# Kernel optimization log

Hardware: AMD Instinct MI355X
Metric: run time of the kernel (lower is better)

Reference implementation:

```python
import jax, jax.numpy as jnp
import numpy as np

# Module config (matches init_kwargs)
N_HEADS = 32        # query heads
MAX_SEQLEN = 2048
LOCAL_BLOCKS = 16
VERT_STRIDE = 8
BLOCK_SIZE = 64
HEAD_SIZE = 128
KV_HEADS = 8
BATCH = 2
SEQLEN = 1024       # per-sample length (equal-length varlen batch)


def _dense_sparse_mask(maxlen):
    """Local + strided block-sparse causal mask, heterogeneous heads.
    Returns bool [N_HEADS, maxlen, maxlen]; True = attend."""
    nb = MAX_SEQLEN // BLOCK_SIZE
    q_pos = jnp.arange(nb)[:, None]
    k_pos = jnp.arange(nb)[None, :]
    h = jnp.arange(N_HEADS)[:, None]
    # head-dependent vertical stride (homo_head=False)
    vert = ((jnp.arange(nb)[None, :] + h + 1) % VERT_STRIDE == 0)  # [H, nb]
    blk = (q_pos >= k_pos) & (((q_pos - k_pos) < LOCAL_BLOCKS)[None] | vert[:, None, :])  # [H, nb, nb]
    tok = jnp.repeat(jnp.repeat(blk, BLOCK_SIZE, axis=1), BLOCK_SIZE, axis=2)  # [H, S, S]
    causal = jnp.tril(jnp.ones((MAX_SEQLEN, MAX_SEQLEN), dtype=bool))
    tok = tok & causal[None]
    return tok[:, :maxlen, :maxlen]


def setup_inputs() -> dict:
    key = jax.random.key(0)
    kq, kk, kv = jax.random.split(key, 3)
    total = BATCH * SEQLEN
    q = jax.random.normal(kq, (total, N_HEADS, HEAD_SIZE), dtype=jnp.float32)
    k = jax.random.normal(kk, (total, KV_HEADS, HEAD_SIZE), dtype=jnp.float32)
    v = jax.random.normal(kv, (total, KV_HEADS, HEAD_SIZE), dtype=jnp.float32)
    cu_seqlens_k = jnp.arange(BATCH + 1, dtype=jnp.int32) * SEQLEN  # [0, 1024, 2048]
    return {"q": q, "k": k, "v": v, "cu_seqlens_k": cu_seqlens_k}


def reference(q, k, v, cu_seqlens_k):
    B = cu_seqlens_k.shape[0] - 1
    T, Hq, D = q.shape
    Hk = k.shape[1]
    r = Hq // Hk                      # q/kv head ratio (GQA)
    L = T // B                        # equal-length sequences
    scale = 1.0 / np.sqrt(D)

    mask = _dense_sparse_mask(L)      # [Hq, L, L]
    bias = jnp.where(mask, jnp.float32(0.0), jnp.finfo(jnp.float32).min)
    bias = bias.reshape(Hk, r, L, L)

    qb = q.reshape(B, L, Hk, r, D)
    kb = k.reshape(B, L, Hk, D)
    vb = v.reshape(B, L, Hk, D)

    scores = jnp.einsum('bqgrd,bkgd->bgrqk', qb, kb) * scale  # [B, Hk, r, L, L]
    attn = jax.nn.softmax(scores + bias[None], axis=-1)
    out = jnp.einsum('bgrqk,bkgd->bqgrd', attn, vb)           # [B, L, Hk, r, D]
    return out.reshape(T, Hq, D)
```

## Files before the change

### kernel.cpp

```cpp
#include <hip/hip_runtime.h>

typedef __attribute__((ext_vector_type(8))) short s8bf;
typedef __attribute__((ext_vector_type(4))) float f4;
typedef __attribute__((ext_vector_type(2))) unsigned u2;
typedef __attribute__((ext_vector_type(4))) unsigned u4;

#define HQ 32
#define HK 8
#define DH 128

static __device__ __forceinline__ unsigned cvtpk(float a, float b) {
  unsigned r;
  asm("v_cvt_pk_bf16_f32 %0, %1, %2" : "=v"(r) : "v"(a), "v"(b));
  return r;
}
union frag_u { s8bf v; unsigned u[4]; };

static __device__ __forceinline__ void gload_lds16(const short* g, short* l) {
  __builtin_amdgcn_global_load_lds(
      (const __attribute__((address_space(1))) void*)g,
      (__attribute__((address_space(3))) void*)l, 16, 0, 0);
}

#define WAIT_VM(N)                                         \
  do {                                                     \
    asm volatile("s_waitcnt vmcnt(" #N ")" ::: "memory");  \
    __builtin_amdgcn_sched_barrier(0);                     \
  } while (0)


__global__ void prep_kernel(const float* __restrict__ kg, const float* __restrict__ vg,
                            short* __restrict__ kbt, short* __restrict__ vbt) {
  const int blk = blockIdx.x;
  if (blk < 512) {
    const int gid = blk * 256 + threadIdx.x;
#pragma unroll
    for (int i = 0; i < 2; ++i) {
      int c = gid + i * 131072;
      int l16 = c & 15, quad = (c >> 4) & 3;
      int f = (c >> 6) & 15;
      int kt = (c >> 10) & 15;
      int bg = c >> 14;
      int b = bg >> 3, g = bg & 7;
      int key = kt * 64 + (f >> 2) * 16 + l16;
      int d0 = (f & 3) * 32 + quad * 8;
      const float* src = kg + (((size_t)(b * 1024 + key) * HK + g) * DH + d0);
      f4 a = *(const f4*)src, cc = *(const f4*)(src + 4);
      u4 w;
      w[0] = cvtpk(a[0], a[1]);   w[1] = cvtpk(a[2], a[3]);
      w[2] = cvtpk(cc[0], cc[1]); w[3] = cvtpk(cc[2], cc[3]);
      *(u4*)(kbt + (size_t)c * 8) = w;
    }
  } else {
    __shared__ short T[32 * 130];
    const int t = blk - 512;
    const int half = t & 1, tile = t >> 1;
    const int bg = tile >> 4, kt = tile & 15;
    const int b = bg >> 3, g = bg & 7;
#pragma unroll
    for (int i = 0; i < 4; ++i) {
      int e = threadIdx.x * 4 + i * 1024;
      int key = e >> 7, d = e & 127;
      f4 x = *(const f4*)(vg + (((size_t)(b * 1024 + kt * 64 + half * 32 + key) * HK + g) * DH + d));
      u2 w; w[0] = cvtpk(x[0], x[1]); w[1] = cvtpk(x[2], x[3]);
      *(u2*)&T[key * 130 + d] = w;
    }
    __syncthreads();
    short* dst = vbt + (size_t)(bg * 16 + kt) * 8192;
#pragma unroll
    for (int i = 0; i < 2; ++i) {
      int c = threadIdx.x + i * 256;
      int lane = c & 63, dt = c >> 6;
      int fidx = dt * 2 + half;
      int l16 = lane & 15, quad = (lane >> 4) & 3;
      int d = dt * 16 + l16;
      int k0 = quad * 4;
      int k1 = k0 + 16;
      u4 w;
      w[0] = (unsigned)(unsigned short)T[(k0 + 0) * 130 + d] |
             ((unsigned)(unsigned short)T[(k0 + 1) * 130 + d] << 16);
      w[1] = (unsigned)(unsigned short)T[(k0 + 2) * 130 + d] |
             ((unsigned)(unsigned short)T[(k0 + 3) * 130 + d] << 16);
      w[2] = (unsigned)(unsigned short)T[(k1 + 0) * 130 + d] |
             ((unsigned)(unsigned short)T[(k1 + 1) * 130 + d] << 16);
      w[3] = (unsigned)(unsigned short)T[(k1 + 2) * 130 + d] |
             ((unsigned)(unsigned short)T[(k1 + 3) * 130 + d] << 16);
      *(u4*)(dst + (size_t)(fidx * 64 + lane) * 8) = w;
    }
  }
}

__launch_bounds__(256, 4)
__global__ void fa_main(const float* __restrict__ qg, const short* __restrict__ kbt,
                        const short* __restrict__ vbt, float* __restrict__ out) {
  const int id  = blockIdx.x;
  const int g   = id & 7;
  const int s   = id >> 3;
  const int qt  = 15 - (s >> 3);
  const int rem = s & 7;
  const int b   = rem >> 2;
  const int h   = g * 4 + (rem & 3);
  const int bg  = b * 8 + g;
  const int kmax = 2 * qt + 1;

  const int tid  = threadIdx.x;
  const int wave = tid >> 6, lane = tid & 63;
  const int l16  = lane & 15, quad = lane >> 4;
  const int qlocal = wave * 16 + l16;
  const int seq0 = b * 1024;

  __shared__ short smem[2][8192];

  const float qmul = 0.08838834764831845f * 1.4426950408889634f;
  const float* qp = qg + ((size_t)(seq0 + qt * 64 + qlocal) * HQ + h) * DH;
  s8bf qf[4];
#pragma unroll
  for (int dk = 0; dk < 4; ++dk) {
    const float* p = qp + dk * 32 + quad * 8;
    f4 a = *(const f4*)p, c = *(const f4*)(p + 4);
    frag_u t;
    t.u[0] = cvtpk(a[0] * qmul, a[1] * qmul);
    t.u[1] = cvtpk(a[2] * qmul, a[3] * qmul);
    t.u[2] = cvtpk(c[0] * qmul, c[1] * qmul);
    t.u[3] = cvtpk(c[2] * qmul, c[3] * qmul);
    qf[dk] = t.v;
  }

  float l_ = 0.0f;
  f4 oacc[8];
#pragma unroll
  for (int dt = 0; dt < 8; ++dt) oacc[dt] = (f4)(0.0f);

  const short* ktile = kbt + (size_t)bg * 16 * 8192;
  const short* vtile = vbt + (size_t)bg * 16 * 8192;

  __builtin_amdgcn_sched_barrier(0);

#define STAGE_TILE(J, BUF)                                                             \
  do {                                                                                 \
    const short* kb32 = ktile + (size_t)((J) >> 1) * 8192 + ((J) & 1) * 4096;          \
    const short* vb32 = vtile + (size_t)((J) >> 1) * 8192 + ((J) & 1) * 512;           \
    _Pragma("unroll")                                                                  \
    for (int i = 0; i < 4; ++i) {                                                      \
      int fidx = wave * 4 + i;                                                         \
      if (fidx < 8) {                                                                  \
        gload_lds16(kb32 + (size_t)(fidx * 64 + lane) * 8, &smem[BUF][fidx * 512]);    \
      } else {                                                                         \
        gload_lds16(vb32 + (size_t)((fidx - 8) * 128 + lane) * 8,                      \
                    &smem[BUF][4096 + (fidx - 8) * 512]);                              \
      }                                                                                \
    }                                                                                  \
  } while (0)

  STAGE_TILE(0, 0);

  for (int kt = 0; kt <= kmax; ++kt) {
    const int cur = kt & 1;

    if (kt < kmax) {
      STAGE_TILE(kt + 1, cur ^ 1);
      WAIT_VM(4);
    } else {
      WAIT_VM(0);
    }
    __builtin_amdgcn_s_barrier();
    __builtin_amdgcn_sched_barrier(0);

    const short* kb = &smem[cur][lane * 8];
    const short* vb = &smem[cur][4096 + lane * 8];

    f4 sacc[2];
#pragma unroll
    for (int ct = 0; ct < 2; ++ct) sacc[ct] = (f4)(0.0f);
    __builtin_amdgcn_s_setprio(1);
#pragma unroll
    for (int dk = 0; dk < 4; ++dk)
#pragma unroll
      for (int ct = 0; ct < 2; ++ct) {
        s8bf kf = *(const s8bf*)&kb[(ct * 4 + dk) * 512];
        sacc[ct] = __builtin_amdgcn_mfma_f32_16x16x32_bf16(kf, qf[dk], sacc[ct], 0, 0, 0);
      }
    __builtin_amdgcn_s_setprio(0);

    if (kt >= 2 * qt) {
      int thr = qlocal - (kt - 2 * qt) * 32;
#pragma unroll
      for (int ct = 0; ct < 2; ++ct)
#pragma unroll
        for (int i = 0; i < 4; ++i) {
          int key = ct * 16 + quad * 4 + i;
          if (key > thr) sacc[ct][i] = -1e30f;
        }
    }

    float rs = 0.0f;
    frag_u fr;
#pragma unroll
    for (int ct = 0; ct < 2; ++ct) {
      float p0 = exp2f(fminf(sacc[ct][0], 30.0f));
      float p1 = exp2f(fminf(sacc[ct][1], 30.0f));
      float p2 = exp2f(fminf(sacc[ct][2], 30.0f));
      float p3 = exp2f(fminf(sacc[ct][3], 30.0f));
      rs += (p0 + p1) + (p2 + p3);
      fr.u[ct * 2 + 0] = cvtpk(p0, p1);
      fr.u[ct * 2 + 1] = cvtpk(p2, p3);
    }
    l_ += rs;

    __builtin_amdgcn_s_setprio(1);
#pragma unroll
    for (int dt = 0; dt < 8; ++dt) {
      s8bf vf = *(const s8bf*)&vb[dt * 512];
      oacc[dt] = __builtin_amdgcn_mfma_f32_16x16x32_bf16(vf, fr.v, oacc[dt], 0, 0, 0);
    }
    __builtin_amdgcn_s_setprio(0);

    asm volatile("s_waitcnt lgkmcnt(0)" ::: "memory");
    __builtin_amdgcn_sched_barrier(0);
    __builtin_amdgcn_s_barrier();
  }

  float lt = l_;
  lt += __shfl_xor(lt, 16);
  lt += __shfl_xor(lt, 32);
  float inv = 1.0f / lt;
  float* op = out + ((size_t)(seq0 + qt * 64 + qlocal) * HQ + h) * DH;
#pragma unroll
  for (int dt = 0; dt < 8; ++dt) {
    f4 w;
    w[0] = oacc[dt][0] * inv; w[1] = oacc[dt][1] * inv;
    w[2] = oacc[dt][2] * inv; w[3] = oacc[dt][3] * inv;
    *(f4*)(op + dt * 16 + quad * 4) = w;
  }
}

extern "C" void kernel_launch(void* const* d_in, const int* in_sizes, int n_in,
                              void* d_out, int out_size, void* d_ws, size_t ws_size,
                              hipStream_t stream) {
  const float* q = (const float*)d_in[0];
  const float* k = (const float*)d_in[1];
  const float* v = (const float*)d_in[2];
  float* out = (float*)d_out;

  short* kbt = (short*)d_ws;
  short* vbt = kbt + (size_t)16 * 16 * 8192;

  prep_kernel<<<dim3(1024), 256, 0, stream>>>(k, v, kbt, vbt);
  fa_main<<<dim3(1024), 256, 0, stream>>>(q, kbt, vbt, out);
}
```

Baseline: 125.2 us.

## Software-pipeline QK^T of next tile with softmax and PV of current tile

```diff
diff --git a/kernel.cpp b/kernel.cpp
--- a/kernel.cpp
+++ b/kernel.cpp
@@ -90,7 +90,7 @@
   }
 }
 
-__launch_bounds__(256, 4)
+__launch_bounds__(256, 3)
 __global__ void fa_main(const float* __restrict__ qg, const short* __restrict__ kbt,
                         const short* __restrict__ vbt, float* __restrict__ out) {
   const int id  = blockIdx.x;
@@ -109,7 +109,7 @@
   const int qlocal = wave * 16 + l16;
   const int seq0 = b * 1024;
 
-  __shared__ short smem[2][8192];
+  __shared__ short smem[3][8192];
 
   const float qmul = 0.08838834764831845f * 1.4426950408889634f;
   const float* qp = qg + ((size_t)(seq0 + qt * 64 + qlocal) * HQ + h) * DH;
@@ -152,72 +152,91 @@
     }                                                                                  \
   } while (0)
 
+#define COMPUTE_S(SACC, BUF, J)                                                        \
+  do {                                                                                 \
+    const short* kb = &smem[BUF][lane * 8];                                            \
+    _Pragma("unroll")                                                                  \
+    for (int ct = 0; ct < 2; ++ct) (SACC)[ct] = (f4)(0.0f);                            \
+    __builtin_amdgcn_s_setprio(1);                                                     \
+    _Pragma("unroll")                                                                  \
+    for (int dk = 0; dk < 4; ++dk)                                                     \
+      _Pragma("unroll")                                                                \
+      for (int ct = 0; ct < 2; ++ct) {                                                 \
+        s8bf kf = *(const s8bf*)&kb[(ct * 4 + dk) * 512];                              \
+        (SACC)[ct] = __builtin_amdgcn_mfma_f32_16x16x32_bf16(kf, qf[dk], (SACC)[ct], 0, 0, 0); \
+      }                                                                                \
+    __builtin_amdgcn_s_setprio(0);                                                     \
+    if ((J) >= 2 * qt) {                                                               \
+      int thr = qlocal - ((J) - 2 * qt) * 32;                                          \
+      _Pragma("unroll")                                                                \
+      for (int ct = 0; ct < 2; ++ct)                                                   \
+        _Pragma("unroll")                                                              \
+        for (int i = 0; i < 4; ++i) {                                                  \
+          int key = ct * 16 + quad * 4 + i;                                            \
+          if (key > thr) (SACC)[ct][i] = -1e30f;                                       \
+        }                                                                              \
+    }                                                                                  \
+  } while (0)
+
   STAGE_TILE(0, 0);
-
-  for (int kt = 0; kt <= kmax; ++kt) {
-    const int cur = kt & 1;
-
-    if (kt < kmax) {
-      STAGE_TILE(kt + 1, cur ^ 1);
-      WAIT_VM(4);
-    } else {
-      WAIT_VM(0);
-    }
-    __builtin_amdgcn_s_barrier();
-    __builtin_amdgcn_sched_barrier(0);
-
-    const short* kb = &smem[cur][lane * 8];
-    const short* vb = &smem[cur][4096 + lane * 8];
-
-    f4 sacc[2];
-#pragma unroll
-    for (int ct = 0; ct < 2; ++ct) sacc[ct] = (f4)(0.0f);
-    __builtin_amdgcn_s_setprio(1);
-#pragma unroll
-    for (int dk = 0; dk < 4; ++dk)
-#pragma unroll
-      for (int ct = 0; ct < 2; ++ct) {
-        s8bf kf = *(const s8bf*)&kb[(ct * 4 + dk) * 512];
-        sacc[ct] = __builtin_amdgcn_mfma_f32_16x16x32_bf16(kf, qf[dk], sacc[ct], 0, 0, 0);
-      }
-    __builtin_amdgcn_s_setprio(0);
-
-    if (kt >= 2 * qt) {
-      int thr = qlocal - (kt - 2 * qt) * 32;
-#pragma unroll
-      for (int ct = 0; ct < 2; ++ct)
-#pragma unroll
-        for (int i = 0; i < 4; ++i) {
-          int key = ct * 16 + quad * 4 + i;
-          if (key > thr) sacc[ct][i] = -1e30f;
-        }
+  WAIT_VM(0);
+  __builtin_amdgcn_s_barrier();
+  __builtin_amdgcn_sched_barrier(0);
+  STAGE_TILE(1, 1);
+
+  f4 saccC[2];
+  COMPUTE_S(saccC, 0, 0);
+
+  for (int t = 0; t <= kmax; ++t) {
+    const int bc = t % 3;
+
+    s8bf vfr[8];
+    {
+      const short* vb = &smem[bc][4096 + lane * 8];
+#pragma unroll
+      for (int dt = 0; dt < 8; ++dt) vfr[dt] = *(const s8bf*)&vb[dt * 512];
     }
 
     float rs = 0.0f;
     frag_u fr;
 #pragma unroll
     for (int ct = 0; ct < 2; ++ct) {
-      float p0 = exp2f(fminf(sacc[ct][0], 30.0f));
-      float p1 = exp2f(fminf(sacc[ct][1], 30.0f));
-      float p2 = exp2f(fminf(sacc[ct][2], 30.0f));
-      float p3 = exp2f(fminf(sacc[ct][3], 30.0f));
+      float p0 = exp2f(fminf(saccC[ct][0], 30.0f));
+      float p1 = exp2f(fminf(saccC[ct][1], 30.0f));
+      float p2 = exp2f(fminf(saccC[ct][2], 30.0f));
+      float p3 = exp2f(fminf(saccC[ct][3], 30.0f));
       rs += (p0 + p1) + (p2 + p3);
       fr.u[ct * 2 + 0] = cvtpk(p0, p1);
       fr.u[ct * 2 + 1] = cvtpk(p2, p3);
     }
     l_ += rs;
 
+    f4 saccN[2];
+    if (t < kmax) {
+      if (t + 2 <= kmax) {
+        STAGE_TILE(t + 2, (t + 2) % 3);
+        WAIT_VM(4);
+      } else {
+        WAIT_VM(0);
+      }
+      __builtin_amdgcn_s_barrier();
+      __builtin_amdgcn_sched_barrier(0);
+      COMPUTE_S(saccN, (t + 1) % 3, t + 1);
+    }
+
     __builtin_amdgcn_s_setprio(1);
 #pragma unroll
-    for (int dt = 0; dt < 8; ++dt) {
-      s8bf vf = *(const s8bf*)&vb[dt * 512];
-      oacc[dt] = __builtin_amdgcn_mfma_f32_16x16x32_bf16(vf, fr.v, oacc[dt], 0, 0, 0);
-    }
+    for (int dt = 0; dt < 8; ++dt)
+      oacc[dt] = __builtin_amdgcn_mfma_f32_16x16x32_bf16(vfr[dt], fr.v, oacc[dt], 0, 0, 0);
     __builtin_amdgcn_s_setprio(0);
 
-    asm volatile("s_waitcnt lgkmcnt(0)" ::: "memory");
-    __builtin_amdgcn_sched_barrier(0);
-    __builtin_amdgcn_s_barrier();
+    if (t < kmax) {
+      asm volatile("s_waitcnt lgkmcnt(0)" ::: "memory");
+      __builtin_amdgcn_sched_barrier(0);
+      __builtin_amdgcn_s_barrier();
+      saccC[0] = saccN[0];
+      saccC[1] = saccN[1];
+    }
   }
 
   float lt = l_;
```

Result: slower. 129.1 us (+3.1%).

## Split key range across two wave groups per block and merge partials via LDS

Applied to the files above, without the earlier changes.

```diff
diff --git a/kernel.cpp b/kernel.cpp
--- a/kernel.cpp
+++ b/kernel.cpp
@@ -90,7 +90,7 @@
   }
 }
 
-__launch_bounds__(256, 4)
+__launch_bounds__(512, 4)
 __global__ void fa_main(const float* __restrict__ qg, const short* __restrict__ kbt,
                         const short* __restrict__ vbt, float* __restrict__ out) {
   const int id  = blockIdx.x;
@@ -101,15 +101,15 @@
   const int b   = rem >> 2;
   const int h   = g * 4 + (rem & 3);
   const int bg  = b * 8 + g;
-  const int kmax = 2 * qt + 1;
 
   const int tid  = threadIdx.x;
   const int wave = tid >> 6, lane = tid & 63;
+  const int half = wave >> 2, wsub = wave & 3;
   const int l16  = lane & 15, quad = lane >> 4;
-  const int qlocal = wave * 16 + l16;
+  const int qlocal = wsub * 16 + l16;
   const int seq0 = b * 1024;
 
-  __shared__ short smem[2][8192];
+  __shared__ short smem[2][2][8192];
 
   const float qmul = 0.08838834764831845f * 1.4426950408889634f;
   const float* qp = qg + ((size_t)(seq0 + qt * 64 + qlocal) * HQ + h) * DH;
@@ -142,23 +142,27 @@
     const short* vb32 = vtile + (size_t)((J) >> 1) * 8192 + ((J) & 1) * 512;           \
     _Pragma("unroll")                                                                  \
     for (int i = 0; i < 4; ++i) {                                                      \
-      int fidx = wave * 4 + i;                                                         \
+      int fidx = wsub * 4 + i;                                                         \
       if (fidx < 8) {                                                                  \
-        gload_lds16(kb32 + (size_t)(fidx * 64 + lane) * 8, &smem[BUF][fidx * 512]);    \
+        gload_lds16(kb32 + (size_t)(fidx * 64 + lane) * 8,                             \
+                    &smem[half][BUF][fidx * 512]);                                     \
       } else {                                                                         \
         gload_lds16(vb32 + (size_t)((fidx - 8) * 128 + lane) * 8,                      \
-                    &smem[BUF][4096 + (fidx - 8) * 512]);                              \
+                    &smem[half][BUF][4096 + (fidx - 8) * 512]);                        \
       }                                                                                \
     }                                                                                  \
   } while (0)
 
-  STAGE_TILE(0, 0);
-
-  for (int kt = 0; kt <= kmax; ++kt) {
-    const int cur = kt & 1;
-
-    if (kt < kmax) {
-      STAGE_TILE(kt + 1, cur ^ 1);
+  STAGE_TILE(half, 0);
+  WAIT_VM(0);
+  __builtin_amdgcn_s_barrier();
+  __builtin_amdgcn_sched_barrier(0);
+
+  for (int j = 0; j <= qt; ++j) {
+    const int cur = j & 1;
+
+    if (j < qt) {
+      STAGE_TILE(2 * (j + 1) + half, cur ^ 1);
       WAIT_VM(4);
     } else {
       WAIT_VM(0);
@@ -166,8 +170,8 @@
     __builtin_amdgcn_s_barrier();
     __builtin_amdgcn_sched_barrier(0);
 
-    const short* kb = &smem[cur][lane * 8];
-    const short* vb = &smem[cur][4096 + lane * 8];
+    const short* kb = &smem[half][cur][lane * 8];
+    const short* vb = &smem[half][cur][4096 + lane * 8];
 
     f4 sacc[2];
 #pragma unroll
@@ -182,8 +186,8 @@
       }
     __builtin_amdgcn_s_setprio(0);
 
-    if (kt >= 2 * qt) {
-      int thr = qlocal - (kt - 2 * qt) * 32;
+    if (j == qt) {
+      int thr = qlocal - half * 32;
 #pragma unroll
       for (int ct = 0; ct < 2; ++ct)
 #pragma unroll
@@ -197,10 +201,10 @@
     frag_u fr;
 #pragma unroll
     for (int ct = 0; ct < 2; ++ct) {
-      float p0 = exp2f(fminf(sacc[ct][0], 30.0f));
-      float p1 = exp2f(fminf(sacc[ct][1], 30.0f));
-      float p2 = exp2f(fminf(sacc[ct][2], 30.0f));
-      float p3 = exp2f(fminf(sacc[ct][3], 30.0f));
+      float p0 = exp2f(sacc[ct][0]);
+      float p1 = exp2f(sacc[ct][1]);
+      float p2 = exp2f(sacc[ct][2]);
+      float p3 = exp2f(sacc[ct][3]);
       rs += (p0 + p1) + (p2 + p3);
       fr.u[ct * 2 + 0] = cvtpk(p0, p1);
       fr.u[ct * 2 + 1] = cvtpk(p2, p3);
@@ -220,17 +224,34 @@
     __builtin_amdgcn_s_barrier();
   }
 
-  float lt = l_;
-  lt += __shfl_xor(lt, 16);
-  lt += __shfl_xor(lt, 32);
-  float inv = 1.0f / lt;
-  float* op = out + ((size_t)(seq0 + qt * 64 + qlocal) * HQ + h) * DH;
-#pragma unroll
-  for (int dt = 0; dt < 8; ++dt) {
-    f4 w;
-    w[0] = oacc[dt][0] * inv; w[1] = oacc[dt][1] * inv;
-    w[2] = oacc[dt][2] * inv; w[3] = oacc[dt][3] * inv;
-    *(f4*)(op + dt * 16 + quad * 4) = w;
+  float* mb = (float*)&smem[0][0][0];
+  const int mrow = wsub * 64 + lane;
+  if (half == 1) {
+#pragma unroll
+    for (int dt = 0; dt < 8; ++dt) *(f4*)&mb[mrow * 36 + dt * 4] = oacc[dt];
+    mb[mrow * 36 + 32] = l_;
+  }
+  __syncthreads();
+  if (half == 0) {
+#pragma unroll
+    for (int dt = 0; dt < 8; ++dt) {
+      f4 p = *(const f4*)&mb[mrow * 36 + dt * 4];
+      oacc[dt][0] += p[0]; oacc[dt][1] += p[1];
+      oacc[dt][2] += p[2]; oacc[dt][3] += p[3];
+    }
+    l_ += mb[mrow * 36 + 32];
+    float lt = l_;
+    lt += __shfl_xor(lt, 16);
+    lt += __shfl_xor(lt, 32);
+    float inv = 1.0f / lt;
+    float* op = out + ((size_t)(seq0 + qt * 64 + qlocal) * HQ + h) * DH;
+#pragma unroll
+    for (int dt = 0; dt < 8; ++dt) {
+      f4 w;
+      w[0] = oacc[dt][0] * inv; w[1] = oacc[dt][1] * inv;
+      w[2] = oacc[dt][2] * inv; w[3] = oacc[dt][3] * inv;
+      *(f4*)(op + dt * 16 + quad * 4) = w;
+    }
   }
 }
 
@@ -246,5 +267,5 @@
   short* vbt = kbt + (size_t)16 * 16 * 8192;
 
   prep_kernel<<<dim3(1024), 256, 0, stream>>>(k, v, kbt, vbt);
-  fa_main<<<dim3(1024), 256, 0, stream>>>(q, kbt, vbt, out);
-}
+  fa_main<<<dim3(1024), 512, 0, stream>>>(q, kbt, vbt, out);
+}
```

New measurement: 127.8 us. 2.0% more time.
